# Kernel optimization log

Measured on AMD Instinct MI355X. Metric: run time of the kernel, lower is better.

Reference implementation:

```python
import jax, jax.numpy as jnp
import numpy as np
import math

N_HEADS = 16

def _rope_tables(seq_len, half_dim, theta=10000.0):
    inv = 1.0 / (theta ** (np.arange(0, half_dim, dtype=np.float32) / half_dim))
    ang = np.arange(seq_len, dtype=np.float32)[:, None] * inv[None, :]
    return jnp.asarray(np.cos(ang)), jnp.asarray(np.sin(ang))

def setup_inputs() -> dict:
    key = jax.random.key(0)
    ks = jax.random.split(key, 5)
    B, S, D = 2, 2048, 2048
    x = jax.random.normal(ks[0], (B, S, D), dtype=jnp.float32)
    scale = 0.02
    wq = jax.random.normal(ks[1], (D, D), dtype=jnp.float32) * scale
    wk = jax.random.normal(ks[2], (D, D), dtype=jnp.float32) * scale
    wv = jax.random.normal(ks[3], (D, D), dtype=jnp.float32) * scale
    wo = jax.random.normal(ks[4], (D, D), dtype=jnp.float32) * scale
    head_dim = D // N_HEADS
    freqs_cos, freqs_sin = _rope_tables(S, head_dim // 2)  # [S, head_dim/2]
    return {"x": x, "wq": wq, "wk": wk, "wv": wv, "wo": wo,
            "freqs_cos": freqs_cos, "freqs_sin": freqs_sin}

def _apply_rope(t, cos, sin):
    # t: [B,S,H,Dh]; pairs (even, odd) along last dim treated as complex
    b, s, h, dh = t.shape
    tr = t.reshape(b, s, h, dh // 2, 2)
    re, im = tr[..., 0], tr[..., 1]
    c = cos[None, :, None, :]
    sn = sin[None, :, None, :]
    out_re = re * c - im * sn
    out_im = re * sn + im * c
    return jnp.stack([out_re, out_im], axis=-1).reshape(b, s, h, dh)

def reference(x, wq, wk, wv, wo, freqs_cos, freqs_sin):
    b, s, dim = x.shape
    h = N_HEADS
    dh = dim // h
    xq = (x @ wq.T).reshape(b, s, h, dh)
    xk = (x @ wk.T).reshape(b, s, h, dh)
    xv = (x @ wv.T).reshape(b, s, h, dh)
    xq = _apply_rope(xq, freqs_cos, freqs_sin)
    xk = _apply_rope(xk, freqs_cos, freqs_sin)
    # n_rep == 1 -> keys/values used directly (matches torch repeat_kv fast path)
    scores = jnp.einsum('bqhd,bkhd->bhqk', xq, xk) / math.sqrt(dh)
    scores = jax.nn.softmax(scores.astype(jnp.float32), axis=-1).astype(xq.dtype)
    # Faithful to torch einsum 'itkl,imtn->itkn': l and m are summed SEPARATELY
    # (no contraction between attn weights kv-axis and values seq-axis).
    out = jnp.einsum('bhql,bmhn->bhqn', scores, xv)  # [B,H,S,Dh]
    out = out.transpose(0, 2, 1, 3).reshape(b, s, dim)
    return out @ wo.T
```

## Files before the change

kernel.cpp:

```cpp
#include <hip/hip_runtime.h>

#define SEQ 2048
#define DM  2048

__global__ __launch_bounds__(256)
void colsum_part(const float* __restrict__ x, float* __restrict__ P) {
    int c = blockIdx.x * blockDim.x + threadIdx.x;
    int y = blockIdx.y;
    int b = blockIdx.z;
    const float* p = x + ((size_t)b * SEQ + (size_t)y * 128) * DM + c;
    float acc = 0.f;
#pragma unroll 8
    for (int r = 0; r < 128; ++r) acc += p[(size_t)r * DM];
    P[(b * 16 + y) * DM + c] = acc;
}

__global__ __launch_bounds__(256)
void colsum_final(const float* __restrict__ P, float* __restrict__ xsum) {
    int c = blockIdx.x * blockDim.x + threadIdx.x;
    int b = blockIdx.y;
    float a = 0.f;
#pragma unroll
    for (int y = 0; y < 16; ++y) a += P[(b * 16 + y) * DM + c];
    xsum[b * DM + c] = a;
}

__global__ __launch_bounds__(256)
void matvec_nt(const float* __restrict__ v, const float* __restrict__ W,
               float* __restrict__ o) {
    int w    = threadIdx.x >> 6;
    int lane = threadIdx.x & 63;
    int n = blockIdx.x * 4 + w;
    int b = blockIdx.y;
    const float4* wr = (const float4*)(W + (size_t)n * DM);
    const float4* vr = (const float4*)(v + (size_t)b * DM);
    float acc = 0.f;
#pragma unroll
    for (int i = lane; i < DM / 4; i += 64) {
        float4 a = wr[i];
        float4 xx = vr[i];
        acc += a.x * xx.x + a.y * xx.y + a.z * xx.z + a.w * xx.w;
    }
#pragma unroll
    for (int m = 32; m; m >>= 1) acc += __shfl_xor(acc, m, 64);
    if (lane == 0) o[b * DM + n] = acc;
}

__global__ __launch_bounds__(256)
void bcast_out(const float* __restrict__ r, float* __restrict__ out, int n4) {
    int i = blockIdx.x * blockDim.x + threadIdx.x;
    if (i >= n4) return;
    int b  = (i >= (SEQ * DM / 4)) ? 1 : 0;
    int j4 = i & (DM / 4 - 1);
    ((float4*)out)[i] = ((const float4*)r)[b * (DM / 4) + j4];
}

extern "C" void kernel_launch(void* const* d_in, const int* in_sizes, int n_in,
                              void* d_out, int out_size, void* d_ws, size_t ws_size,
                              hipStream_t stream) {
    const float* x  = (const float*)d_in[0];
    const float* wv = (const float*)d_in[3];
    const float* wo = (const float*)d_in[4];
    float* out = (float*)d_out;

    float* ws   = (float*)d_ws;
    float* P    = ws;
    float* xsum = P + 32 * DM;
    float* sv   = xsum + 2 * DM;
    float* rr   = sv + 2 * DM;

    colsum_part <<<dim3(DM / 256, 16, 2), 256, 0, stream>>>(x, P);
    colsum_final<<<dim3(DM / 256, 2),     256, 0, stream>>>(P, xsum);
    matvec_nt   <<<dim3(DM / 4, 2),       256, 0, stream>>>(xsum, wv, sv);
    matvec_nt   <<<dim3(DM / 4, 2),       256, 0, stream>>>(sv, wo, rr);

    int n4 = 2 * SEQ * DM / 4;
    bcast_out   <<<dim3(n4 / 256),        256, 0, stream>>>(rr, out, n4);
}
```

Baseline: 33.31 us.

## Vectorize column-sum, batch both rows in matvec, use nontemporal loads/stores

The column-sum partial kernel now reads float4 vectors with nontemporal loads and splits the sequence into 64 chunks of 32 rows instead of 16 chunks of 128, giving more independent blocks; the final reduction sums 64 partials. The matvec kernel processes both batch rows per weight load, so each weight matrix is read once instead of twice. The broadcast kernel drops its bounds check and uses nontemporal stores. These changes target memory bandwidth on the x read, the weight reads and the large output write, at the cost of a larger partial buffer and more work in the final reduction.

```diff
diff --git a/kernel.cpp b/kernel.cpp
--- a/kernel.cpp
+++ b/kernel.cpp
@@ -3,56 +3,67 @@
 #define SEQ 2048
 #define DM  2048
 
+typedef float f4 __attribute__((ext_vector_type(4)));
+
 __global__ __launch_bounds__(256)
 void colsum_part(const float* __restrict__ x, float* __restrict__ P) {
-    int c = blockIdx.x * blockDim.x + threadIdx.x;
-    int y = blockIdx.y;
-    int b = blockIdx.z;
-    const float* p = x + ((size_t)b * SEQ + (size_t)y * 128) * DM + c;
-    float acc = 0.f;
-#pragma unroll 8
-    for (int r = 0; r < 128; ++r) acc += p[(size_t)r * DM];
-    P[(b * 16 + y) * DM + c] = acc;
+    int c4 = blockIdx.x * 256 + threadIdx.x;
+    int y  = blockIdx.y;
+    int b  = blockIdx.z;
+    const f4* p = (const f4*)(x + ((size_t)b * SEQ + (size_t)y * 32) * DM) + c4;
+    f4 acc = {0.f, 0.f, 0.f, 0.f};
+#pragma unroll
+    for (int r = 0; r < 32; ++r) {
+        f4 v = __builtin_nontemporal_load(&p[(size_t)r * (DM / 4)]);
+        acc += v;
+    }
+    ((f4*)(P + ((size_t)b * 64 + y) * DM))[c4] = acc;
 }
 
 __global__ __launch_bounds__(256)
 void colsum_final(const float* __restrict__ P, float* __restrict__ xsum) {
-    int c = blockIdx.x * blockDim.x + threadIdx.x;
+    int c = blockIdx.x * 256 + threadIdx.x;
     int b = blockIdx.y;
+    const float* p = P + (size_t)b * 64 * DM + c;
     float a = 0.f;
 #pragma unroll
-    for (int y = 0; y < 16; ++y) a += P[(b * 16 + y) * DM + c];
+    for (int y = 0; y < 64; ++y) a += p[(size_t)y * DM];
     xsum[b * DM + c] = a;
 }
 
 __global__ __launch_bounds__(256)
-void matvec_nt(const float* __restrict__ v, const float* __restrict__ W,
-               float* __restrict__ o) {
+void matvec2(const float* __restrict__ v, const float* __restrict__ W,
+             float* __restrict__ o) {
     int w    = threadIdx.x >> 6;
     int lane = threadIdx.x & 63;
     int n = blockIdx.x * 4 + w;
-    int b = blockIdx.y;
-    const float4* wr = (const float4*)(W + (size_t)n * DM);
-    const float4* vr = (const float4*)(v + (size_t)b * DM);
-    float acc = 0.f;
+    const f4* wr = (const f4*)(W + (size_t)n * DM);
+    const f4* v0 = (const f4*)v;
+    const f4* v1 = (const f4*)(v + DM);
+    float a0 = 0.f, a1 = 0.f;
 #pragma unroll
     for (int i = lane; i < DM / 4; i += 64) {
-        float4 a = wr[i];
-        float4 xx = vr[i];
-        acc += a.x * xx.x + a.y * xx.y + a.z * xx.z + a.w * xx.w;
+        f4 a = __builtin_nontemporal_load(&wr[i]);
+        f4 p = v0[i];
+        f4 q = v1[i];
+        a0 += a.x * p.x + a.y * p.y + a.z * p.z + a.w * p.w;
+        a1 += a.x * q.x + a.y * q.y + a.z * q.z + a.w * q.w;
     }
 #pragma unroll
-    for (int m = 32; m; m >>= 1) acc += __shfl_xor(acc, m, 64);
-    if (lane == 0) o[b * DM + n] = acc;
+    for (int m = 32; m; m >>= 1) {
+        a0 += __shfl_xor(a0, m, 64);
+        a1 += __shfl_xor(a1, m, 64);
+    }
+    if (lane == 0) { o[n] = a0; o[DM + n] = a1; }
 }
 
 __global__ __launch_bounds__(256)
-void bcast_out(const float* __restrict__ r, float* __restrict__ out, int n4) {
-    int i = blockIdx.x * blockDim.x + threadIdx.x;
-    if (i >= n4) return;
+void bcast_out(const float* __restrict__ r, float* __restrict__ out) {
+    int i  = blockIdx.x * 256 + threadIdx.x;
     int b  = (i >= (SEQ * DM / 4)) ? 1 : 0;
     int j4 = i & (DM / 4 - 1);
-    ((float4*)out)[i] = ((const float4*)r)[b * (DM / 4) + j4];
+    f4 val = ((const f4*)r)[b * (DM / 4) + j4];
+    __builtin_nontemporal_store(val, &((f4*)out)[i]);
 }
 
 extern "C" void kernel_launch(void* const* d_in, const int* in_sizes, int n_in,
@@ -65,15 +76,15 @@
 
     float* ws   = (float*)d_ws;
     float* P    = ws;
-    float* xsum = P + 32 * DM;
+    float* xsum = P + 2 * 64 * DM;
     float* sv   = xsum + 2 * DM;
     float* rr   = sv + 2 * DM;
 
-    colsum_part <<<dim3(DM / 256, 16, 2), 256, 0, stream>>>(x, P);
-    colsum_final<<<dim3(DM / 256, 2),     256, 0, stream>>>(P, xsum);
-    matvec_nt   <<<dim3(DM / 4, 2),       256, 0, stream>>>(xsum, wv, sv);
-    matvec_nt   <<<dim3(DM / 4, 2),       256, 0, stream>>>(sv, wo, rr);
+    colsum_part <<<dim3(2, 64, 2), 256, 0, stream>>>(x, P);
+    colsum_final<<<dim3(8, 2),     256, 0, stream>>>(P, xsum);
+    matvec2     <<<dim3(DM / 4),   256, 0, stream>>>(xsum, wv, sv);
+    matvec2     <<<dim3(DM / 4),   256, 0, stream>>>(sv, wo, rr);
 
     int n4 = 2 * SEQ * DM / 4;
-    bcast_out   <<<dim3(n4 / 256),        256, 0, stream>>>(rr, out, n4);
+    bcast_out   <<<dim3(n4 / 256), 256, 0, stream>>>(rr, out);
 }
```

Measured after the change: 42.21 us. 1.27x slower.
